# Performance work log

Measured on AMD Instinct MI355X. Metric: run time of the kernel, lower is better.

Reference implementation:

```python
import jax, jax.numpy as jnp
import numpy as np

N, E, F_IN, H, D, HID, G = 50000, 800000, 64, 4, 32, 128, 1024
NEG_SLOPE = 0.2


def setup_inputs():
    key = jax.random.key(0)
    ks = jax.random.split(key, 32)
    inp = {
        "x": jax.random.normal(ks[0], (N, F_IN), dtype=jnp.float32),
        "edge_index": jax.random.randint(ks[1], (2, E), 0, N, dtype=jnp.int64),
        "batch": jnp.sort(jax.random.randint(ks[2], (N,), 0, G, dtype=jnp.int64)),
    }
    dims = [F_IN, HID, HID]
    i = 3
    for l, din in enumerate(dims):
        s = 1.0 / np.sqrt(din)
        inp[f"Wl{l}"] = jax.random.normal(ks[i], (din, H * D), dtype=jnp.float32) * s; i += 1
        inp[f"bl{l}"] = jnp.zeros((H * D,), dtype=jnp.float32)
        inp[f"Wr{l}"] = jax.random.normal(ks[i], (din, H * D), dtype=jnp.float32) * s; i += 1
        inp[f"br{l}"] = jnp.zeros((H * D,), dtype=jnp.float32)
        inp[f"att{l}"] = jax.random.normal(ks[i], (H, D), dtype=jnp.float32) * (1.0 / np.sqrt(D)); i += 1
        inp[f"b{l}"] = jnp.zeros((H * D,), dtype=jnp.float32)
    inp["Wh"] = jax.random.normal(ks[i], (HID, 1), dtype=jnp.float32) * (1.0 / np.sqrt(HID))
    inp["bh"] = jnp.zeros((1,), dtype=jnp.float32)
    return inp


def gatv2_layer(x, src, dst, Wl, bl, Wr, br, att, b):
    # GATv2Conv (eval mode, no dropout): e_ij = att . leaky_relu(Wl x_j + Wr x_i)
    xl = (x @ Wl + bl).reshape(-1, H, D)   # source transform
    xr = (x @ Wr + br).reshape(-1, H, D)   # target transform
    m = xl[src] + xr[dst]                  # [E,H,D]
    e = jnp.where(m >= 0, m, NEG_SLOPE * m)
    score = jnp.einsum("ehd,hd->eh", e, att)          # [E,H]
    smax = jax.ops.segment_max(score, dst, num_segments=N)  # [N,H]
    expv = jnp.exp(score - smax[dst])
    denom = jax.ops.segment_sum(expv, dst, num_segments=N)
    alpha = expv / denom[dst]                          # softmax over in-edges of dst
    agg = jax.ops.segment_sum(alpha[:, :, None] * xl[src], dst, num_segments=N)
    return agg.reshape(-1, H * D) + b


def reference(x, edge_index, batch, Wl0, bl0, Wr0, br0, att0, b0,
              Wl1, bl1, Wr1, br1, att1, b1,
              Wl2, bl2, Wr2, br2, att2, b2, Wh, bh):
    src, dst = edge_index[0], edge_index[1]
    params = [(Wl0, bl0, Wr0, br0, att0, b0),
              (Wl1, bl1, Wr1, br1, att1, b1),
              (Wl2, bl2, Wr2, br2, att2, b2)]
    h = x
    for p in params:
        h = gatv2_layer(h, src, dst, *p)
        h = jax.nn.elu(h)  # dropout inactive in eval
    # global mean pool over graphs
    sums = jax.ops.segment_sum(h, batch, num_segments=G)
    cnt = jax.ops.segment_sum(jnp.ones((h.shape[0],), h.dtype), batch, num_segments=G)
    pooled = sums / jnp.maximum(cnt, 1.0)[:, None]
    return pooled @ Wh + bh
```

## Files before the change

kernel.cpp:

```cpp
#include <hip/hip_runtime.h>
#include <math.h>

#define N_NODES 50000
#define N_EDGES 800000
#define HD 128
#define GG 1024
#define NEG_SLOPE 0.2f
#define SCAN_B 1024
#define NB ((N_NODES + SCAN_B - 1) / SCAN_B)

typedef __attribute__((ext_vector_type(8))) short bf16x8;
typedef __attribute__((ext_vector_type(4))) float f32x4;

__device__ __forceinline__ unsigned short f2bf(float v) {
    unsigned u = __float_as_uint(v);
    u += 0x7fff + ((u >> 16) & 1);
    return (unsigned short)(u >> 16);
}
__device__ __forceinline__ float bf2f(unsigned short s) {
    return __uint_as_float((unsigned)s << 16);
}

__global__ void convert_x(const float* __restrict__ x, unsigned short* __restrict__ Xh,
                          unsigned short* __restrict__ Xl, int total)
{
    int i = blockIdx.x * 256 + threadIdx.x;
    if (i >= total) return;
    float v = x[i];
    unsigned short hi = f2bf(v);
    unsigned short lo = f2bf(v - bf2f(hi));
    Xh[i] = hi; Xl[i] = lo;
}

__global__ void convert_w(const float* __restrict__ Wl, const float* __restrict__ Wr,
                          unsigned short* __restrict__ Wth, unsigned short* __restrict__ Wtl,
                          int K)
{
    int t = blockIdx.x * 256 + threadIdx.x;
    if (t >= 256 * K) return;
    int c = t / K, k = t - c * K;
    float v = (c < 128) ? Wl[(size_t)k * 128 + c] : Wr[(size_t)k * 128 + (c - 128)];
    unsigned short hi = f2bf(v);
    unsigned short lo = f2bf(v - bf2f(hi));
    Wth[t] = hi; Wtl[t] = lo;
}

template<int K>
__launch_bounds__(256)
__global__ void gemm_mfma(const unsigned short* __restrict__ Xh, const unsigned short* __restrict__ Xl,
                          const unsigned short* __restrict__ Wth, const unsigned short* __restrict__ Wtl,
                          const float* __restrict__ bl, const float* __restrict__ br,
                          float* __restrict__ Cl, float* __restrict__ Cr, int n)
{
    constexpr int KC = 32;
    constexpr int NCH = K / KC;
    constexpr int XR = 36;
    __shared__ unsigned short XsH[2][64 * XR];
    __shared__ unsigned short XsL[2][64 * XR];
    const int tid  = threadIdx.x;
    const int wave = tid >> 6;
    const int lane = tid & 63;
    const int quad = lane >> 4;
    const int l15  = lane & 15;
    const int row0 = blockIdx.x * 64;

    f32x4 acc[4][4];
    #pragma unroll
    for (int i = 0; i < 4; i++)
        #pragma unroll
        for (int j = 0; j < 4; j++) acc[i][j] = (f32x4){0.f, 0.f, 0.f, 0.f};

    const int sr  = tid >> 2, seg = tid & 3;
    const int srow = row0 + sr;

    {
        uint4 vh = make_uint4(0,0,0,0), vl = make_uint4(0,0,0,0);
        if (srow < n) {
            const size_t go = (size_t)srow * K + seg * 8;
            vh = *(const uint4*)(Xh + go);
            vl = *(const uint4*)(Xl + go);
        }
        *(uint4*)&XsH[0][sr * XR + seg * 8] = vh;
        *(uint4*)&XsL[0][sr * XR + seg * 8] = vl;
    }
    __syncthreads();

    for (int ch = 0; ch < NCH; ch++) {
        const int cur = ch & 1;
        const bool more = (ch + 1 < NCH);
        uint4 nh = make_uint4(0,0,0,0), nl = make_uint4(0,0,0,0);
        if (more && srow < n) {
            const size_t go = (size_t)srow * K + (ch + 1) * KC + seg * 8;
            nh = *(const uint4*)(Xh + go);
            nl = *(const uint4*)(Xl + go);
        }
        bf16x8 bh[4], bo[4];
        #pragma unroll
        for (int nt = 0; nt < 4; nt++) {
            const size_t wo = (size_t)(wave * 64 + nt * 16 + l15) * K + ch * KC + quad * 8;
            bh[nt] = *(const bf16x8*)(Wth + wo);
            bo[nt] = *(const bf16x8*)(Wtl + wo);
        }
        bf16x8 ah[4], al[4];
        #pragma unroll
        for (int mt = 0; mt < 4; mt++) {
            ah[mt] = *(const bf16x8*)&XsH[cur][(mt * 16 + l15) * XR + quad * 8];
            al[mt] = *(const bf16x8*)&XsL[cur][(mt * 16 + l15) * XR + quad * 8];
        }
        #pragma unroll
        for (int nt = 0; nt < 4; nt++) {
            #pragma unroll
            for (int mt = 0; mt < 4; mt++) {
                acc[mt][nt] = __builtin_amdgcn_mfma_f32_16x16x32_bf16(ah[mt], bh[nt], acc[mt][nt], 0, 0, 0);
                acc[mt][nt] = __builtin_amdgcn_mfma_f32_16x16x32_bf16(ah[mt], bo[nt], acc[mt][nt], 0, 0, 0);
                acc[mt][nt] = __builtin_amdgcn_mfma_f32_16x16x32_bf16(al[mt], bh[nt], acc[mt][nt], 0, 0, 0);
            }
        }
        if (more) {
            *(uint4*)&XsH[1 - cur][sr * XR + seg * 8] = nh;
            *(uint4*)&XsL[1 - cur][sr * XR + seg * 8] = nl;
        }
        __syncthreads();
    }

    const bool isL = (wave < 2);
    const int colbase = (wave & 1) * 64;
    const float* bias = isL ? bl : br;
    float* C = isL ? Cl : Cr;
    #pragma unroll
    for (int nt = 0; nt < 4; nt++) {
        const float bv = bias[colbase + nt * 16 + l15];
        #pragma unroll
        for (int mt = 0; mt < 4; mt++) {
            #pragma unroll
            for (int r = 0; r < 4; r++) {
                const int row = row0 + mt * 16 + quad * 4 + r;
                if (row < n)
                    C[(size_t)row * 128 + colbase + nt * 16 + l15] = acc[mt][nt][r] + bv;
            }
        }
    }
}

__global__ void deg_hist(const int* __restrict__ dst, int* __restrict__ deg) {
    int e = blockIdx.x * 256 + threadIdx.x;
    if (e < N_EDGES) atomicAdd(&deg[dst[e]], 1);
}

__launch_bounds__(SCAN_B)
__global__ void scan_block(const int* __restrict__ deg, int* __restrict__ rowptr,
                           int* __restrict__ btot)
{
    __shared__ int s[SCAN_B];
    const int tid = threadIdx.x;
    const int i = blockIdx.x * SCAN_B + tid;
    int v = (i < N_NODES) ? deg[i] : 0;
    s[tid] = v;
    __syncthreads();
    for (int off = 1; off < SCAN_B; off <<= 1) {
        int t = (tid >= off) ? s[tid - off] : 0;
        __syncthreads();
        s[tid] += t;
        __syncthreads();
    }
    if (i < N_NODES) rowptr[i] = s[tid] - v;
    if (tid == SCAN_B - 1) btot[blockIdx.x] = s[SCAN_B - 1];
}

__global__ void scan_btot(const int* __restrict__ btot, int* __restrict__ boff) {
    if (threadIdx.x == 0) {
        int a = 0;
        for (int b = 0; b < NB; b++) { boff[b] = a; a += btot[b]; }
        boff[NB] = a;
    }
}

__global__ void scan_add(const int* __restrict__ boff, int* __restrict__ rowptr,
                         int* __restrict__ cursor)
{
    int i = blockIdx.x * 256 + threadIdx.x;
    if (i < N_NODES) {
        int r = rowptr[i] + boff[i >> 10];
        rowptr[i] = r;
        cursor[i] = r;
    }
    if (i == N_NODES) rowptr[N_NODES] = boff[NB];
}

__global__ void scatter_csr(const int* __restrict__ src, const int* __restrict__ dst,
                            int* __restrict__ cursor, int* __restrict__ csr_src)
{
    int e = blockIdx.x * 256 + threadIdx.x;
    if (e >= N_EDGES) return;
    int pos = atomicAdd(&cursor[dst[e]], 1);
    csr_src[pos] = src[e];
}

__global__ void build_gptr(const int* __restrict__ batch, int* __restrict__ gptr) {
    int i = blockIdx.x * 256 + threadIdx.x;
    if (i > N_NODES) return;
    if (i == 0) {
        for (int g = 0; g <= batch[0]; g++) gptr[g] = 0;
    } else if (i == N_NODES) {
        for (int g = batch[N_NODES - 1] + 1; g <= GG; g++) gptr[g] = N_NODES;
    } else {
        int b0 = batch[i - 1], b1 = batch[i];
        for (int g = b0 + 1; g <= b1; g++) gptr[g] = i;
    }
}

__launch_bounds__(256)
__global__ void node_attn(const float* __restrict__ xl, const float* __restrict__ xr,
                          const int* __restrict__ rowptr, const int* __restrict__ csr_src,
                          const float* __restrict__ att, const float* __restrict__ bvec,
                          unsigned short* __restrict__ Hh, unsigned short* __restrict__ Hl)
{
    const int node = (blockIdx.x * 256 + threadIdx.x) >> 6;
    const int lane = threadIdx.x & 63;
    if (node >= N_NODES) return;
    const int eslot = lane >> 4;
    const int li    = lane & 15;

    const float* xrp = xr + (size_t)node * HD + li * 8;
    const float4 xr0 = *(const float4*)(xrp);
    const float4 xr1 = *(const float4*)(xrp + 4);
    const float4 aw0 = *(const float4*)(att + li * 8);
    const float4 aw1 = *(const float4*)(att + li * 8 + 4);
    const int beg = rowptr[node];
    const int end = rowptr[node + 1];

    float m = -1e30f, l = 0.f;
    float4 a0 = make_float4(0.f, 0.f, 0.f, 0.f);
    float4 a1 = make_float4(0.f, 0.f, 0.f, 0.f);

    int e0 = beg + eslot;
    int s0 = (e0 < end) ? csr_src[e0] : 0;
    const float* rp0 = xl + (size_t)s0 * HD + li * 8;
    float4 v0 = *(const float4*)(rp0);
    float4 v1 = *(const float4*)(rp0 + 4);

    for (int base = beg; base < end; base += 4) {
        const bool valid = (base + eslot) < end;
        float4 n0 = v0, n1 = v1;
        if (base + 4 < end) {
            int e2 = base + 4 + eslot;
            int s2 = (e2 < end) ? csr_src[e2] : 0;
            const float* rp = xl + (size_t)s2 * HD + li * 8;
            n0 = *(const float4*)(rp);
            n1 = *(const float4*)(rp + 4);
        }
        float t, p;
        t = v0.x + xr0.x; t = fmaxf(t, NEG_SLOPE * t); p  = t * aw0.x;
        t = v0.y + xr0.y; t = fmaxf(t, NEG_SLOPE * t); p += t * aw0.y;
        t = v0.z + xr0.z; t = fmaxf(t, NEG_SLOPE * t); p += t * aw0.z;
        t = v0.w + xr0.w; t = fmaxf(t, NEG_SLOPE * t); p += t * aw0.w;
        t = v1.x + xr1.x; t = fmaxf(t, NEG_SLOPE * t); p += t * aw1.x;
        t = v1.y + xr1.y; t = fmaxf(t, NEG_SLOPE * t); p += t * aw1.y;
        t = v1.z + xr1.z; t = fmaxf(t, NEG_SLOPE * t); p += t * aw1.z;
        t = v1.w + xr1.w; t = fmaxf(t, NEG_SLOPE * t); p += t * aw1.w;
        p += __shfl_xor(p, 1);
        p += __shfl_xor(p, 2);

        if (!__any(valid && (p > m))) {
            const float w = valid ? __expf(p - m) : 0.f;
            l += w;
            a0.x += w * v0.x; a0.y += w * v0.y; a0.z += w * v0.z; a0.w += w * v0.w;
            a1.x += w * v1.x; a1.y += w * v1.y; a1.z += w * v1.z; a1.w += w * v1.w;
        } else {
            const float mn = valid ? fmaxf(m, p) : m;
            const float sc = __expf(m - mn);
            const float w  = valid ? __expf(p - mn) : 0.f;
            l = l * sc + w;
            a0.x = a0.x * sc + w * v0.x; a0.y = a0.y * sc + w * v0.y;
            a0.z = a0.z * sc + w * v0.z; a0.w = a0.w * sc + w * v0.w;
            a1.x = a1.x * sc + w * v1.x; a1.y = a1.y * sc + w * v1.y;
            a1.z = a1.z * sc + w * v1.z; a1.w = a1.w * sc + w * v1.w;
            m = mn;
        }
        v0 = n0; v1 = n1;
    }

    #pragma unroll
    for (int off = 16; off <= 32; off <<= 1) {
        const float mo = __shfl_xor(m, off);
        const float lo = __shfl_xor(l, off);
        float4 b0, b1;
        b0.x = __shfl_xor(a0.x, off); b0.y = __shfl_xor(a0.y, off);
        b0.z = __shfl_xor(a0.z, off); b0.w = __shfl_xor(a0.w, off);
        b1.x = __shfl_xor(a1.x, off); b1.y = __shfl_xor(a1.y, off);
        b1.z = __shfl_xor(a1.z, off); b1.w = __shfl_xor(a1.w, off);
        const float mm = fmaxf(m, mo);
        const float e1 = __expf(m - mm);
        const float e2 = __expf(mo - mm);
        l = l * e1 + lo * e2;
        a0.x = a0.x * e1 + b0.x * e2; a0.y = a0.y * e1 + b0.y * e2;
        a0.z = a0.z * e1 + b0.z * e2; a0.w = a0.w * e1 + b0.w * e2;
        a1.x = a1.x * e1 + b1.x * e2; a1.y = a1.y * e1 + b1.y * e2;
        a1.z = a1.z * e1 + b1.z * e2; a1.w = a1.w * e1 + b1.w * e2;
        m = mm;
    }

    if (eslot == 0) {
        const float inv = (l > 0.f) ? 1.f / l : 0.f;
        const float4 bb0 = *(const float4*)(bvec + li * 8);
        const float4 bb1 = *(const float4*)(bvec + li * 8 + 4);
        float o[8];
        o[0] = a0.x * inv + bb0.x; o[1] = a0.y * inv + bb0.y;
        o[2] = a0.z * inv + bb0.z; o[3] = a0.w * inv + bb0.w;
        o[4] = a1.x * inv + bb1.x; o[5] = a1.y * inv + bb1.y;
        o[6] = a1.z * inv + bb1.z; o[7] = a1.w * inv + bb1.w;
        uint4 ph, pl;
        unsigned* php = (unsigned*)&ph;
        unsigned* plp = (unsigned*)&pl;
        #pragma unroll
        for (int j = 0; j < 4; j++) {
            float u0 = o[2*j], u1 = o[2*j+1];
            u0 = (u0 > 0.f) ? u0 : expm1f(u0);
            u1 = (u1 > 0.f) ? u1 : expm1f(u1);
            unsigned short h0 = f2bf(u0), h1 = f2bf(u1);
            unsigned short q0 = f2bf(u0 - bf2f(h0)), q1 = f2bf(u1 - bf2f(h1));
            php[j] = (unsigned)h0 | ((unsigned)h1 << 16);
            plp[j] = (unsigned)q0 | ((unsigned)q1 << 16);
        }
        *(uint4*)(Hh + (size_t)node * HD + li * 8) = ph;
        *(uint4*)(Hl + (size_t)node * HD + li * 8) = pl;
    }
}

__launch_bounds__(256)
__global__ void pool_head(const unsigned short* __restrict__ Hh, const unsigned short* __restrict__ Hl,
                          const int* __restrict__ gptr, const float* __restrict__ Wh,
                          const float* __restrict__ bh, float* __restrict__ out)
{
    const int g = (blockIdx.x * 256 + threadIdx.x) >> 6;
    const int lane = threadIdx.x & 63;
    if (g >= GG) return;
    const int b0 = gptr[g], b1 = gptr[g + 1];
    const float2 w = *(const float2*)(Wh + lane * 2);
    float sx = 0.f, sy = 0.f;
    for (int i = b0; i < b1; i++) {
        const unsigned vh = *(const unsigned*)(Hh + (size_t)i * HD + lane * 2);
        const unsigned vl = *(const unsigned*)(Hl + (size_t)i * HD + lane * 2);
        sx += bf2f((unsigned short)(vh & 0xffff)) + bf2f((unsigned short)(vl & 0xffff));
        sy += bf2f((unsigned short)(vh >> 16))    + bf2f((unsigned short)(vl >> 16));
    }
    float d = sx * w.x + sy * w.y;
    d += __shfl_xor(d, 1);
    d += __shfl_xor(d, 2);
    d += __shfl_xor(d, 4);
    d += __shfl_xor(d, 8);
    d += __shfl_xor(d, 16);
    d += __shfl_xor(d, 32);
    if (lane == 0) out[g] = d / fmaxf((float)(b1 - b0), 1.f) + bh[0];
}

extern "C" void kernel_launch(void* const* d_in, const int* in_sizes, int n_in,
                              void* d_out, int out_size, void* d_ws, size_t ws_size,
                              hipStream_t stream)
{
    const float* x     = (const float*)d_in[0];
    const int*   edge  = (const int*)d_in[1];
    const int*   batch = (const int*)d_in[2];
    const int*   src   = edge;
    const int*   dst   = edge + N_EDGES;
    const float* Wh    = (const float*)d_in[21];
    const float* bh    = (const float*)d_in[22];
    float* out = (float*)d_out;

    const size_t N128 = (size_t)N_NODES * HD;
    float* buf_xl = (float*)d_ws;
    float* buf_xr = buf_xl + N128;
    unsigned short* Xh  = (unsigned short*)(buf_xr + N128);
    unsigned short* Xl_ = Xh + N128;
    unsigned short* Wth = Xl_ + N128;
    unsigned short* Wtl = Wth + 3 * 256 * 128;
    int* deg     = (int*)(Wtl + 3 * 256 * 128);
    int* rowptr  = deg + N_NODES;
    int* cursor  = rowptr + N_NODES + 1;
    int* csr_src = cursor + N_NODES;
    int* btot    = csr_src + N_EDGES;
    int* boff    = btot + NB;
    int* gptr    = boff + NB + 1;

    hipMemsetAsync(deg, 0, (size_t)N_NODES * sizeof(int), stream);
    deg_hist<<<(N_EDGES + 255) / 256, 256, 0, stream>>>(dst, deg);
    scan_block<<<NB, SCAN_B, 0, stream>>>(deg, rowptr, btot);
    scan_btot<<<1, 64, 0, stream>>>(btot, boff);
    scan_add<<<(N_NODES + 256) / 256, 256, 0, stream>>>(boff, rowptr, cursor);
    scatter_csr<<<(N_EDGES + 255) / 256, 256, 0, stream>>>(src, dst, cursor, csr_src);
    build_gptr<<<(N_NODES + 256) / 256, 256, 0, stream>>>(batch, gptr);

    convert_x<<<(N_NODES * 64 + 255) / 256, 256, 0, stream>>>(x, Xh, Xl_, N_NODES * 64);
    for (int l = 0; l < 3; l++) {
        const int K = (l == 0) ? 64 : 128;
        convert_w<<<(256 * K + 255) / 256, 256, 0, stream>>>(
            (const float*)d_in[3 + 6 * l], (const float*)d_in[5 + 6 * l],
            Wth + l * 256 * 128, Wtl + l * 256 * 128, K);
    }

    const int gemm_grid = (N_NODES + 63) / 64;
    const int attn_grid = (N_NODES + 3) / 4;

    for (int l = 0; l < 3; l++) {
        const float* bl  = (const float*)d_in[4 + 6 * l];
        const float* br  = (const float*)d_in[6 + 6 * l];
        const float* att = (const float*)d_in[7 + 6 * l];
        const float* bb  = (const float*)d_in[8 + 6 * l];

        if (l == 0)
            gemm_mfma<64><<<gemm_grid, 256, 0, stream>>>(Xh, Xl_, Wth, Wtl,
                                                         bl, br, buf_xl, buf_xr, N_NODES);
        else
            gemm_mfma<128><<<gemm_grid, 256, 0, stream>>>(Xh, Xl_,
                                                          Wth + l * 256 * 128, Wtl + l * 256 * 128,
                                                          bl, br, buf_xl, buf_xr, N_NODES);
        node_attn<<<attn_grid, 256, 0, stream>>>(buf_xl, buf_xr, rowptr, csr_src,
                                                 att, bb, Xh, Xl_);
    }

    pool_head<<<GG / 4, 256, 0, stream>>>(Xh, Xl_, gptr, Wh, bh, out);
}
```

Baseline: 534.6 us.

## Load GEMM operands directly from global, deepen attention prefetch, merge weight conversions

```diff
diff --git a/kernel.cpp b/kernel.cpp
--- a/kernel.cpp
+++ b/kernel.cpp
@@ -32,17 +32,24 @@
     Xh[i] = hi; Xl[i] = lo;
 }
 
-__global__ void convert_w(const float* __restrict__ Wl, const float* __restrict__ Wr,
-                          unsigned short* __restrict__ Wth, unsigned short* __restrict__ Wtl,
-                          int K)
+__global__ void convert_w_all(const float* __restrict__ W0l, const float* __restrict__ W0r,
+                              const float* __restrict__ W1l, const float* __restrict__ W1r,
+                              const float* __restrict__ W2l, const float* __restrict__ W2r,
+                              unsigned short* __restrict__ Wth, unsigned short* __restrict__ Wtl)
 {
     int t = blockIdx.x * 256 + threadIdx.x;
-    if (t >= 256 * K) return;
-    int c = t / K, k = t - c * K;
+    if (t >= 256 * 64 + 2 * 256 * 128) return;
+    int l, local, K;
+    const float* Wl; const float* Wr;
+    if (t < 256 * 64)            { l = 0; local = t;              K = 64;  Wl = W0l; Wr = W0r; }
+    else if (t < 256 * 64 + 256 * 128) { l = 1; local = t - 256 * 64;  K = 128; Wl = W1l; Wr = W1r; }
+    else                         { l = 2; local = t - 256 * 64 - 256 * 128; K = 128; Wl = W2l; Wr = W2r; }
+    int c = local / K, k = local - c * K;
     float v = (c < 128) ? Wl[(size_t)k * 128 + c] : Wr[(size_t)k * 128 + (c - 128)];
     unsigned short hi = f2bf(v);
     unsigned short lo = f2bf(v - bf2f(hi));
-    Wth[t] = hi; Wtl[t] = lo;
+    Wth[l * 256 * 128 + local] = hi;
+    Wtl[l * 256 * 128 + local] = lo;
 }
 
 template<int K>
@@ -52,11 +59,7 @@
                           const float* __restrict__ bl, const float* __restrict__ br,
                           float* __restrict__ Cl, float* __restrict__ Cr, int n)
 {
-    constexpr int KC = 32;
-    constexpr int NCH = K / KC;
-    constexpr int XR = 36;
-    __shared__ unsigned short XsH[2][64 * XR];
-    __shared__ unsigned short XsL[2][64 * XR];
+    constexpr int NCH = K / 32;
     const int tid  = threadIdx.x;
     const int wave = tid >> 6;
     const int lane = tid & 63;
@@ -70,42 +73,45 @@
         #pragma unroll
         for (int j = 0; j < 4; j++) acc[i][j] = (f32x4){0.f, 0.f, 0.f, 0.f};
 
-    const int sr  = tid >> 2, seg = tid & 3;
-    const int srow = row0 + sr;
-
-    {
-        uint4 vh = make_uint4(0,0,0,0), vl = make_uint4(0,0,0,0);
-        if (srow < n) {
-            const size_t go = (size_t)srow * K + seg * 8;
-            vh = *(const uint4*)(Xh + go);
-            vl = *(const uint4*)(Xl + go);
-        }
-        *(uint4*)&XsH[0][sr * XR + seg * 8] = vh;
-        *(uint4*)&XsL[0][sr * XR + seg * 8] = vl;
-    }
-    __syncthreads();
-
-    for (int ch = 0; ch < NCH; ch++) {
-        const int cur = ch & 1;
-        const bool more = (ch + 1 < NCH);
-        uint4 nh = make_uint4(0,0,0,0), nl = make_uint4(0,0,0,0);
-        if (more && srow < n) {
-            const size_t go = (size_t)srow * K + (ch + 1) * KC + seg * 8;
-            nh = *(const uint4*)(Xh + go);
-            nl = *(const uint4*)(Xl + go);
-        }
-        bf16x8 bh[4], bo[4];
-        #pragma unroll
-        for (int nt = 0; nt < 4; nt++) {
-            const size_t wo = (size_t)(wave * 64 + nt * 16 + l15) * K + ch * KC + quad * 8;
-            bh[nt] = *(const bf16x8*)(Wth + wo);
-            bo[nt] = *(const bf16x8*)(Wtl + wo);
-        }
-        bf16x8 ah[4], al[4];
-        #pragma unroll
-        for (int mt = 0; mt < 4; mt++) {
-            ah[mt] = *(const bf16x8*)&XsH[cur][(mt * 16 + l15) * XR + quad * 8];
-            al[mt] = *(const bf16x8*)&XsL[cur][(mt * 16 + l15) * XR + quad * 8];
+    size_t aoff[4];
+    #pragma unroll
+    for (int mt = 0; mt < 4; mt++) {
+        int r = row0 + mt * 16 + l15;
+        if (r >= n) r = n - 1;
+        aoff[mt] = (size_t)r * K + quad * 8;
+    }
+    size_t boff[4];
+    #pragma unroll
+    for (int nt = 0; nt < 4; nt++)
+        boff[nt] = (size_t)(wave * 64 + nt * 16 + l15) * K + quad * 8;
+
+    bf16x8 ah[4], al[4], bh[4], bo[4];
+    #pragma unroll
+    for (int mt = 0; mt < 4; mt++) {
+        ah[mt] = *(const bf16x8*)(Xh + aoff[mt]);
+        al[mt] = *(const bf16x8*)(Xl + aoff[mt]);
+    }
+    #pragma unroll
+    for (int nt = 0; nt < 4; nt++) {
+        bh[nt] = *(const bf16x8*)(Wth + boff[nt]);
+        bo[nt] = *(const bf16x8*)(Wtl + boff[nt]);
+    }
+
+    #pragma unroll
+    for (int ch = 1; ch <= NCH; ch++) {
+        bf16x8 nah[4], nal[4], nbh[4], nbo[4];
+        if (ch < NCH) {
+            const int ko = ch * 32;
+            #pragma unroll
+            for (int mt = 0; mt < 4; mt++) {
+                nah[mt] = *(const bf16x8*)(Xh + aoff[mt] + ko);
+                nal[mt] = *(const bf16x8*)(Xl + aoff[mt] + ko);
+            }
+            #pragma unroll
+            for (int nt = 0; nt < 4; nt++) {
+                nbh[nt] = *(const bf16x8*)(Wth + boff[nt] + ko);
+                nbo[nt] = *(const bf16x8*)(Wtl + boff[nt] + ko);
+            }
         }
         #pragma unroll
         for (int nt = 0; nt < 4; nt++) {
@@ -116,11 +122,13 @@
                 acc[mt][nt] = __builtin_amdgcn_mfma_f32_16x16x32_bf16(al[mt], bh[nt], acc[mt][nt], 0, 0, 0);
             }
         }
-        if (more) {
-            *(uint4*)&XsH[1 - cur][sr * XR + seg * 8] = nh;
-            *(uint4*)&XsL[1 - cur][sr * XR + seg * 8] = nl;
-        }
-        __syncthreads();
+        if (ch < NCH) {
+            #pragma unroll
+            for (int i = 0; i < 4; i++) {
+                ah[i] = nah[i]; al[i] = nal[i];
+                bh[i] = nbh[i]; bo[i] = nbo[i];
+            }
+        }
     }
 
     const bool isL = (wave < 2);
@@ -233,51 +241,56 @@
     float4 a0 = make_float4(0.f, 0.f, 0.f, 0.f);
     float4 a1 = make_float4(0.f, 0.f, 0.f, 0.f);
 
-    int e0 = beg + eslot;
-    int s0 = (e0 < end) ? csr_src[e0] : 0;
+    int i0 = beg + eslot;
+    int s0 = (i0 < end) ? csr_src[i0] : 0;
     const float* rp0 = xl + (size_t)s0 * HD + li * 8;
-    float4 v0 = *(const float4*)(rp0);
-    float4 v1 = *(const float4*)(rp0 + 4);
+    float4 c0 = *(const float4*)(rp0);
+    float4 c1 = *(const float4*)(rp0 + 4);
+    int i1 = beg + 4 + eslot;
+    int s1 = (i1 < end) ? csr_src[i1] : 0;
+    const float* rp1 = xl + (size_t)s1 * HD + li * 8;
+    float4 p0 = *(const float4*)(rp1);
+    float4 p1 = *(const float4*)(rp1 + 4);
 
     for (int base = beg; base < end; base += 4) {
         const bool valid = (base + eslot) < end;
-        float4 n0 = v0, n1 = v1;
-        if (base + 4 < end) {
-            int e2 = base + 4 + eslot;
+        float4 r0 = p0, r1 = p1;
+        if (base + 8 < end) {
+            int e2 = base + 8 + eslot;
             int s2 = (e2 < end) ? csr_src[e2] : 0;
             const float* rp = xl + (size_t)s2 * HD + li * 8;
-            n0 = *(const float4*)(rp);
-            n1 = *(const float4*)(rp + 4);
+            r0 = *(const float4*)(rp);
+            r1 = *(const float4*)(rp + 4);
         }
         float t, p;
-        t = v0.x + xr0.x; t = fmaxf(t, NEG_SLOPE * t); p  = t * aw0.x;
-        t = v0.y + xr0.y; t = fmaxf(t, NEG_SLOPE * t); p += t * aw0.y;
-        t = v0.z + xr0.z; t = fmaxf(t, NEG_SLOPE * t); p += t * aw0.z;
-        t = v0.w + xr0.w; t = fmaxf(t, NEG_SLOPE * t); p += t * aw0.w;
-        t = v1.x + xr1.x; t = fmaxf(t, NEG_SLOPE * t); p += t * aw1.x;
-        t = v1.y + xr1.y; t = fmaxf(t, NEG_SLOPE * t); p += t * aw1.y;
-        t = v1.z + xr1.z; t = fmaxf(t, NEG_SLOPE * t); p += t * aw1.z;
-        t = v1.w + xr1.w; t = fmaxf(t, NEG_SLOPE * t); p += t * aw1.w;
+        t = c0.x + xr0.x; t = fmaxf(t, NEG_SLOPE * t); p  = t * aw0.x;
+        t = c0.y + xr0.y; t = fmaxf(t, NEG_SLOPE * t); p += t * aw0.y;
+        t = c0.z + xr0.z; t = fmaxf(t, NEG_SLOPE * t); p += t * aw0.z;
+        t = c0.w + xr0.w; t = fmaxf(t, NEG_SLOPE * t); p += t * aw0.w;
+        t = c1.x + xr1.x; t = fmaxf(t, NEG_SLOPE * t); p += t * aw1.x;
+        t = c1.y + xr1.y; t = fmaxf(t, NEG_SLOPE * t); p += t * aw1.y;
+        t = c1.z + xr1.z; t = fmaxf(t, NEG_SLOPE * t); p += t * aw1.z;
+        t = c1.w + xr1.w; t = fmaxf(t, NEG_SLOPE * t); p += t * aw1.w;
         p += __shfl_xor(p, 1);
         p += __shfl_xor(p, 2);
 
         if (!__any(valid && (p > m))) {
             const float w = valid ? __expf(p - m) : 0.f;
             l += w;
-            a0.x += w * v0.x; a0.y += w * v0.y; a0.z += w * v0.z; a0.w += w * v0.w;
-            a1.x += w * v1.x; a1.y += w * v1.y; a1.z += w * v1.z; a1.w += w * v1.w;
+            a0.x += w * c0.x; a0.y += w * c0.y; a0.z += w * c0.z; a0.w += w * c0.w;
+            a1.x += w * c1.x; a1.y += w * c1.y; a1.z += w * c1.z; a1.w += w * c1.w;
         } else {
             const float mn = valid ? fmaxf(m, p) : m;
             const float sc = __expf(m - mn);
             const float w  = valid ? __expf(p - mn) : 0.f;
             l = l * sc + w;
-            a0.x = a0.x * sc + w * v0.x; a0.y = a0.y * sc + w * v0.y;
-            a0.z = a0.z * sc + w * v0.z; a0.w = a0.w * sc + w * v0.w;
-            a1.x = a1.x * sc + w * v1.x; a1.y = a1.y * sc + w * v1.y;
-            a1.z = a1.z * sc + w * v1.z; a1.w = a1.w * sc + w * v1.w;
+            a0.x = a0.x * sc + w * c0.x; a0.y = a0.y * sc + w * c0.y;
+            a0.z = a0.z * sc + w * c0.z; a0.w = a0.w * sc + w * c0.w;
+            a1.x = a1.x * sc + w * c1.x; a1.y = a1.y * sc + w * c1.y;
+            a1.z = a1.z * sc + w * c1.z; a1.w = a1.w * sc + w * c1.w;
             m = mn;
         }
-        v0 = n0; v1 = n1;
+        c0 = p0; c1 = p1; p0 = r0; p1 = r1;
     }
 
     #pragma unroll
@@ -391,12 +404,10 @@
     build_gptr<<<(N_NODES + 256) / 256, 256, 0, stream>>>(batch, gptr);
 
     convert_x<<<(N_NODES * 64 + 255) / 256, 256, 0, stream>>>(x, Xh, Xl_, N_NODES * 64);
-    for (int l = 0; l < 3; l++) {
-        const int K = (l == 0) ? 64 : 128;
-        convert_w<<<(256 * K + 255) / 256, 256, 0, stream>>>(
-            (const float*)d_in[3 + 6 * l], (const float*)d_in[5 + 6 * l],
-            Wth + l * 256 * 128, Wtl + l * 256 * 128, K);
-    }
+    convert_w_all<<<(256 * 64 + 2 * 256 * 128 + 255) / 256, 256, 0, stream>>>(
+        (const float*)d_in[3],  (const float*)d_in[5],
+        (const float*)d_in[9],  (const float*)d_in[11],
+        (const float*)d_in[15], (const float*)d_in[17], Wth, Wtl);
 
     const int gemm_grid = (N_NODES + 63) / 64;
     const int attn_grid = (N_NODES + 3) / 4;
```

After: 549.6 us. 1.03x slower.
